# Performance work log

Measured on AMD Instinct MI355X. Metric: run time of the kernel, lower is better.

Reference implementation:

```python
import jax, jax.numpy as jnp
import numpy as np

B, N, D = 1024, 8192, 128
BETA = 0.25


def setup_inputs() -> dict:
    key = jax.random.key(0)
    kx, kw = jax.random.split(key)
    x = jax.random.normal(kx, (B, D), dtype=jnp.float32)
    # nn.Embedding weight init: uniform(-1/num_embeddings, 1/num_embeddings)
    W = jax.random.uniform(kw, (N, D), dtype=jnp.float32, minval=-1.0 / N, maxval=1.0 / N)
    return {"x": x, "W": W}


def reference(x, W):
    # Squared L2 distances: (B, N) via expansion; single GEMM for the cross term.
    dist = (x * x).sum(axis=1, keepdims=True) - 2.0 * (x @ W.T) + (W * W).sum(axis=1)[None, :]
    # (-dist).topk(k=1) == argmin(dist); torch keeps the k dim -> ind is (B, 1)
    ind = jnp.argmin(dist, axis=1)[:, None]
    q = W[ind]  # (B, 1, D) codebook gather (matches torch embedding(ind) shape)
    # Faithful to source: (B, D) broadcasts against (B, 1, D) -> (B, B, D)
    loss = BETA * jnp.mean((x - jax.lax.stop_gradient(q)) ** 2) + jnp.mean((jax.lax.stop_gradient(x) - q) ** 2)
    quantized = x + jax.lax.stop_gradient(q - x)  # straight-through; (B, B, D) per source broadcast
    return quantized, ind, loss
```

## Files before the change

kernel.cpp:

```cpp
#include <hip/hip_runtime.h>
#include <stdint.h>

typedef float vfloat4 __attribute__((ext_vector_type(4)));

static const long long QN       = 134217728LL;
static const long long IND_OFF  = QN;
static const long long LOSS_OFF = QN + 1024;

#define WS_W2    0
#define WS_X2    8192
#define WS_SX    9216
#define WS_SQ    9344
#define WS_SQ2   9472
#define WS_PVAL  16384
#define WS_PIDX  81920
#define WS_Q     147456

__global__ __launch_bounds__(256) void k_prep(const float* __restrict__ x,
                                              const float* __restrict__ W,
                                              float* __restrict__ ws) {
    const int b = blockIdx.x, tid = threadIdx.x;
    if (b < 36) {
        const float4* pr = (b < 32) ? ((const float4*)W + (size_t)(b * 256 + tid) * 32)
                                    : ((const float4*)x + (size_t)((b - 32) * 256 + tid) * 32);
        float s = 0.0f;
#pragma unroll 8
        for (int t = 0; t < 32; ++t) {
            float4 v = pr[t];
            s += v.x * v.x + v.y * v.y + v.z * v.z + v.w * v.w;
        }
        if (b < 32) ws[WS_W2 + b * 256 + tid] = s;
        else        ws[WS_X2 + (b - 32) * 256 + tid] = s;
    } else {
        __shared__ float sh[8][32];
        const int c = tid & 31, g = tid >> 5;
        const int col = (b - 36) * 32 + c;
        float sum = 0.0f;
        for (int r = g; r < 1024; r += 8) sum += x[(size_t)r * 128 + col];
        sh[g][c] = sum;
        __syncthreads();
        if (g == 0) {
            float t = 0.0f;
#pragma unroll
            for (int gg = 0; gg < 8; ++gg) t += sh[gg][c];
            ws[WS_SX + col] = t;
        }
        if (b == 36 && tid < 129) ws[WS_SQ + tid] = 0.0f;
    }
}

__global__ __launch_bounds__(256) void k_score(
    const float* __restrict__ x, const float* __restrict__ W,
    const float* __restrict__ w2, const float* __restrict__ x2,
    float* __restrict__ pval, int* __restrict__ pidx) {
    __shared__ float Xs[32][132];
    __shared__ float Wst[32][132];
    const int tid = threadIdx.x;
    const int tx = tid & 15, ty = tid >> 4;
    const int n0 = blockIdx.x * 128, m0 = blockIdx.y * 128;
    const float4* xv = (const float4*)x;
    const float4* wv = (const float4*)W;

    float acc[8][8];
#pragma unroll
    for (int i = 0; i < 8; ++i)
#pragma unroll
        for (int j = 0; j < 8; ++j) acc[i][j] = 0.0f;

    for (int kc = 0; kc < 4; ++kc) {
#pragma unroll
        for (int it = 0; it < 4; ++it) {
            int f = it * 256 + tid;
            int m = f >> 3, kq = f & 7;
            float4 a = xv[(size_t)(m0 + m) * 32 + kc * 8 + kq];
            float4 b = wv[(size_t)(n0 + m) * 32 + kc * 8 + kq];
            Xs[kq * 4 + 0][m] = a.x;
            Xs[kq * 4 + 1][m] = a.y;
            Xs[kq * 4 + 2][m] = a.z;
            Xs[kq * 4 + 3][m] = a.w;
            Wst[kq * 4 + 0][m] = b.x;
            Wst[kq * 4 + 1][m] = b.y;
            Wst[kq * 4 + 2][m] = b.z;
            Wst[kq * 4 + 3][m] = b.w;
        }
        __syncthreads();
#pragma unroll 8
        for (int k = 0; k < 32; ++k) {
            float4 a0 = *(const float4*)&Xs[k][ty * 8];
            float4 a1 = *(const float4*)&Xs[k][ty * 8 + 4];
            float4 b0 = *(const float4*)&Wst[k][tx * 8];
            float4 b1 = *(const float4*)&Wst[k][tx * 8 + 4];
            float af[8] = {a0.x, a0.y, a0.z, a0.w, a1.x, a1.y, a1.z, a1.w};
            float bf[8] = {b0.x, b0.y, b0.z, b0.w, b1.x, b1.y, b1.z, b1.w};
#pragma unroll
            for (int i = 0; i < 8; ++i)
#pragma unroll
                for (int j = 0; j < 8; ++j) acc[i][j] += af[i] * bf[j];
        }
        __syncthreads();
    }

    float w2v[8];
#pragma unroll
    for (int j = 0; j < 8; ++j) w2v[j] = w2[n0 + tx * 8 + j];

#pragma unroll
    for (int i = 0; i < 8; ++i) {
        const int row = m0 + ty * 8 + i;
        const float xxv = x2[row];
        float bestv;
        int besti = n0 + tx * 8;
        {
            float t = xxv - 2.0f * acc[i][0];
            bestv = t + w2v[0];
        }
#pragma unroll
        for (int j = 1; j < 8; ++j) {
            float t = xxv - 2.0f * acc[i][j];
            float s = t + w2v[j];
            if (s < bestv) { bestv = s; besti = n0 + tx * 8 + j; }
        }
        for (int off = 1; off < 16; off <<= 1) {
            float ov = __shfl_xor(bestv, off, 64);
            int oi = __shfl_xor(besti, off, 64);
            if (ov < bestv || (ov == bestv && oi < besti)) { bestv = ov; besti = oi; }
        }
        if (tx == 0) {
            pval[row * 64 + blockIdx.x] = bestv;
            pidx[row * 64 + blockIdx.x] = besti;
        }
    }
}

__global__ __launch_bounds__(256) void k_argmin(
    const float* __restrict__ W, const float* __restrict__ w2,
    const float* __restrict__ pval, const int* __restrict__ pidx,
    float* __restrict__ out, float* __restrict__ ws) {
    __shared__ int sidx[256];
    __shared__ float sh[2][128];
    const int tid = threadIdx.x;
    const int r = blockIdx.x * 256 + tid;
    float bestv = pval[r * 64];
    int besti = pidx[r * 64];
    for (int c = 1; c < 64; ++c) {
        float v = pval[r * 64 + c];
        if (v < bestv) { bestv = v; besti = pidx[r * 64 + c]; }
    }
    out[IND_OFF + r] = (float)besti;
    sidx[tid] = besti;

    float q2 = w2[besti];
    for (int off = 1; off < 64; off <<= 1) q2 += __shfl_xor(q2, off, 64);
    if ((tid & 63) == 0) atomicAdd(ws + WS_SQ2, q2);
    __syncthreads();

    const int c4 = tid & 31, rg = tid >> 5;
    float4* wsq = (float4*)(ws + WS_Q);
    const float4* wv = (const float4*)W;
#pragma unroll 4
    for (int it = 0; it < 32; ++it) {
        int rr = it * 8 + rg;
        int idx = sidx[rr];
        wsq[(size_t)(blockIdx.x * 256 + rr) * 32 + c4] = wv[(size_t)idx * 32 + c4];
    }

    const int d = tid & 127, g = tid >> 7;
    float s = 0.0f;
    for (int rr = g; rr < 256; rr += 2) s += W[(size_t)sidx[rr] * 128 + d];
    sh[g][d] = s;
    __syncthreads();
    if (g == 0) atomicAdd(ws + WS_SQ + d, sh[0][d] + sh[1][d]);
}

__global__ __launch_bounds__(256) void k_bcast(float* __restrict__ out,
                                               const float* __restrict__ ws) {
    const int bid = blockIdx.x, tid = threadIdx.x;
    if (bid == 0) {
        __shared__ float sh[256];
        float dotv = (tid < 128) ? ws[WS_SX + tid] * ws[WS_SQ + tid] : 0.0f;
        float sx2 = 0.0f;
        for (int r = tid; r < 1024; r += 256) sx2 += ws[WS_X2 + r];
        sh[tid] = dotv;
        __syncthreads();
        for (int s = 128; s > 0; s >>= 1) {
            if (tid < s) sh[tid] += sh[tid + s];
            __syncthreads();
        }
        const float dot = sh[0];
        __syncthreads();
        sh[tid] = sx2;
        __syncthreads();
        for (int s = 128; s > 0; s >>= 1) {
            if (tid < s) sh[tid] += sh[tid + s];
            __syncthreads();
        }
        if (tid == 0) {
            double Sx2 = (double)sh[0], Sq2 = (double)ws[WS_SQ2];
            double loss = 1.25 * (1024.0 * Sx2 + 1024.0 * Sq2 - 2.0 * (double)dot) / 134217728.0;
            out[LOSS_OFF] = (float)loss;
        }
        __syncthreads();
    }
    const int i = bid >> 3;
    const int e = bid & 7;
    const int t = tid & 31;
    const vfloat4* src = (const vfloat4*)(ws + WS_Q) + (size_t)i * 32;
    vfloat4 qv = src[t];
    vfloat4* dst = (vfloat4*)out + (size_t)i * 32768 + t;
    const int jend = e * 128 + 128;
    for (int j = e * 128 + (tid >> 5); j < jend; j += 8) {
        dst[(size_t)j * 32] = qv;
    }
}

extern "C" void kernel_launch(void* const* d_in, const int* in_sizes, int n_in,
                              void* d_out, int out_size, void* d_ws, size_t ws_size,
                              hipStream_t stream) {
    const float* x = (const float*)d_in[0];
    const float* W = (const float*)d_in[1];
    float* out = (float*)d_out;
    float* ws = (float*)d_ws;

    hipLaunchKernelGGL(k_prep, dim3(40), dim3(256), 0, stream, x, W, ws);
    hipLaunchKernelGGL(k_score, dim3(64, 8), dim3(256), 0, stream, x, W,
                       ws + WS_W2, ws + WS_X2, ws + WS_PVAL, (int*)(ws + WS_PIDX));
    hipLaunchKernelGGL(k_argmin, dim3(4), dim3(256), 0, stream, W, ws + WS_W2,
                       ws + WS_PVAL, (const int*)(ws + WS_PIDX), out, ws);
    hipLaunchKernelGGL(k_bcast, dim3(8192), dim3(256), 0, stream, out, ws);
}
```

Measured before the change: 638.7 us.

## Parallelize argmin reduction, use packed FMA in scoring, and batch broadcast blocks

The final argmin now uses one wavefront per row with shuffle reductions across 512 blocks, where before it used 4 blocks with a serial 64-element scan per thread. The loss sums (codebook row sums and squared norms) move into block 0 of the broadcast kernel, which removes the atomics. The score GEMM accumulates in float2 vectors via elementwise fma so the compiler can emit packed FMA instructions. The broadcast kernel now gives each block 4 chunks, using 2049 blocks instead of 8192, with a dedicated loss block that adds a serial 1024-row reduction.

New measurement: 770.5 us. 20.6% more time.

```diff
diff --git a/kernel.cpp b/kernel.cpp
--- a/kernel.cpp
+++ b/kernel.cpp
@@ -2,6 +2,7 @@
 #include <stdint.h>
 
 typedef float vfloat4 __attribute__((ext_vector_type(4)));
+typedef float vfloat2 __attribute__((ext_vector_type(2)));
 
 static const long long QN       = 134217728LL;
 static const long long IND_OFF  = QN;
@@ -10,8 +11,7 @@
 #define WS_W2    0
 #define WS_X2    8192
 #define WS_SX    9216
-#define WS_SQ    9344
-#define WS_SQ2   9472
+#define WS_IND   9344
 #define WS_PVAL  16384
 #define WS_PIDX  81920
 #define WS_Q     147456
@@ -45,10 +45,10 @@
             for (int gg = 0; gg < 8; ++gg) t += sh[gg][c];
             ws[WS_SX + col] = t;
         }
-        if (b == 36 && tid < 129) ws[WS_SQ + tid] = 0.0f;
-    }
-}
-
+    }
+}
+
+#define ACC(i, j) acc[i][(j) >> 1][(j) & 1]
 __global__ __launch_bounds__(256) void k_score(
     const float* __restrict__ x, const float* __restrict__ W,
     const float* __restrict__ w2, const float* __restrict__ x2,
@@ -61,11 +61,11 @@
     const float4* xv = (const float4*)x;
     const float4* wv = (const float4*)W;
 
-    float acc[8][8];
+    vfloat2 acc[8][4];
 #pragma unroll
     for (int i = 0; i < 8; ++i)
 #pragma unroll
-        for (int j = 0; j < 8; ++j) acc[i][j] = 0.0f;
+        for (int jp = 0; jp < 4; ++jp) acc[i][jp] = (vfloat2)(0.0f);
 
     for (int kc = 0; kc < 4; ++kc) {
 #pragma unroll
@@ -91,11 +91,19 @@
             float4 b0 = *(const float4*)&Wst[k][tx * 8];
             float4 b1 = *(const float4*)&Wst[k][tx * 8 + 4];
             float af[8] = {a0.x, a0.y, a0.z, a0.w, a1.x, a1.y, a1.z, a1.w};
-            float bf[8] = {b0.x, b0.y, b0.z, b0.w, b1.x, b1.y, b1.z, b1.w};
-#pragma unroll
-            for (int i = 0; i < 8; ++i)
-#pragma unroll
-                for (int j = 0; j < 8; ++j) acc[i][j] += af[i] * bf[j];
+            vfloat2 bb[4];
+            bb[0][0] = b0.x; bb[0][1] = b0.y;
+            bb[1][0] = b0.z; bb[1][1] = b0.w;
+            bb[2][0] = b1.x; bb[2][1] = b1.y;
+            bb[3][0] = b1.z; bb[3][1] = b1.w;
+#pragma unroll
+            for (int i = 0; i < 8; ++i) {
+                vfloat2 av;
+                av[0] = af[i]; av[1] = af[i];
+#pragma unroll
+                for (int jp = 0; jp < 4; ++jp)
+                    acc[i][jp] = __builtin_elementwise_fma(av, bb[jp], acc[i][jp]);
+            }
         }
         __syncthreads();
     }
@@ -111,12 +119,12 @@
         float bestv;
         int besti = n0 + tx * 8;
         {
-            float t = xxv - 2.0f * acc[i][0];
+            float t = xxv - 2.0f * ACC(i, 0);
             bestv = t + w2v[0];
         }
 #pragma unroll
         for (int j = 1; j < 8; ++j) {
-            float t = xxv - 2.0f * acc[i][j];
+            float t = xxv - 2.0f * ACC(i, j);
             float s = t + w2v[j];
             if (s < bestv) { bestv = s; besti = n0 + tx * 8 + j; }
         }
@@ -132,84 +140,91 @@
     }
 }
 
-__global__ __launch_bounds__(256) void k_argmin(
-    const float* __restrict__ W, const float* __restrict__ w2,
+__global__ __launch_bounds__(128) void k_argmin(
+    const float* __restrict__ W,
     const float* __restrict__ pval, const int* __restrict__ pidx,
     float* __restrict__ out, float* __restrict__ ws) {
-    __shared__ int sidx[256];
-    __shared__ float sh[2][128];
     const int tid = threadIdx.x;
-    const int r = blockIdx.x * 256 + tid;
-    float bestv = pval[r * 64];
-    int besti = pidx[r * 64];
-    for (int c = 1; c < 64; ++c) {
-        float v = pval[r * 64 + c];
-        if (v < bestv) { bestv = v; besti = pidx[r * 64 + c]; }
-    }
-    out[IND_OFF + r] = (float)besti;
-    sidx[tid] = besti;
-
-    float q2 = w2[besti];
-    for (int off = 1; off < 64; off <<= 1) q2 += __shfl_xor(q2, off, 64);
-    if ((tid & 63) == 0) atomicAdd(ws + WS_SQ2, q2);
-    __syncthreads();
-
-    const int c4 = tid & 31, rg = tid >> 5;
-    float4* wsq = (float4*)(ws + WS_Q);
-    const float4* wv = (const float4*)W;
-#pragma unroll 4
-    for (int it = 0; it < 32; ++it) {
-        int rr = it * 8 + rg;
-        int idx = sidx[rr];
-        wsq[(size_t)(blockIdx.x * 256 + rr) * 32 + c4] = wv[(size_t)idx * 32 + c4];
-    }
-
-    const int d = tid & 127, g = tid >> 7;
-    float s = 0.0f;
-    for (int rr = g; rr < 256; rr += 2) s += W[(size_t)sidx[rr] * 128 + d];
-    sh[g][d] = s;
-    __syncthreads();
-    if (g == 0) atomicAdd(ws + WS_SQ + d, sh[0][d] + sh[1][d]);
+    const int w = tid >> 6, lane = tid & 63;
+    const int r = blockIdx.x * 2 + w;
+    float bestv = pval[r * 64 + lane];
+    int besti = pidx[r * 64 + lane];
+    for (int off = 1; off < 64; off <<= 1) {
+        float ov = __shfl_xor(bestv, off, 64);
+        int oi = __shfl_xor(besti, off, 64);
+        if (ov < bestv || (ov == bestv && oi < besti)) { bestv = ov; besti = oi; }
+    }
+    if (lane == 0) {
+        out[IND_OFF + r] = (float)besti;
+        ((int*)ws)[WS_IND + r] = besti;
+    }
+    if (lane < 32) {
+        const float4* wv = (const float4*)W;
+        float4* wsq = (float4*)(ws + WS_Q);
+        wsq[(size_t)r * 32 + lane] = wv[(size_t)besti * 32 + lane];
+    }
 }
 
 __global__ __launch_bounds__(256) void k_bcast(float* __restrict__ out,
                                                const float* __restrict__ ws) {
     const int bid = blockIdx.x, tid = threadIdx.x;
     if (bid == 0) {
+        __shared__ float shq[2][128];
         __shared__ float sh[256];
-        float dotv = (tid < 128) ? ws[WS_SX + tid] * ws[WS_SQ + tid] : 0.0f;
+        const int d = tid & 127, g = tid >> 7;
+        float s = 0.0f;
+        for (int r = g; r < 1024; r += 2) s += ws[WS_Q + (size_t)r * 128 + d];
+        shq[g][d] = s;
+        __syncthreads();
+        float dotv = 0.0f;
+        if (tid < 128) dotv = (shq[0][tid] + shq[1][tid]) * ws[WS_SX + tid];
         float sx2 = 0.0f;
         for (int r = tid; r < 1024; r += 256) sx2 += ws[WS_X2 + r];
+        const int* wsI = (const int*)ws + WS_IND;
+        float sq2 = 0.0f;
+        for (int r = tid; r < 1024; r += 256) sq2 += ws[WS_W2 + wsI[r]];
         sh[tid] = dotv;
         __syncthreads();
-        for (int s = 128; s > 0; s >>= 1) {
-            if (tid < s) sh[tid] += sh[tid + s];
+        for (int st = 128; st > 0; st >>= 1) {
+            if (tid < st) sh[tid] += sh[tid + st];
             __syncthreads();
         }
         const float dot = sh[0];
         __syncthreads();
         sh[tid] = sx2;
         __syncthreads();
-        for (int s = 128; s > 0; s >>= 1) {
-            if (tid < s) sh[tid] += sh[tid + s];
+        for (int st = 128; st > 0; st >>= 1) {
+            if (tid < st) sh[tid] += sh[tid + st];
             __syncthreads();
         }
+        const float Sx2 = sh[0];
+        __syncthreads();
+        sh[tid] = sq2;
+        __syncthreads();
+        for (int st = 128; st > 0; st >>= 1) {
+            if (tid < st) sh[tid] += sh[tid + st];
+            __syncthreads();
+        }
         if (tid == 0) {
-            double Sx2 = (double)sh[0], Sq2 = (double)ws[WS_SQ2];
-            double loss = 1.25 * (1024.0 * Sx2 + 1024.0 * Sq2 - 2.0 * (double)dot) / 134217728.0;
+            double loss = 1.25 * (1024.0 * (double)Sx2 + 1024.0 * (double)sh[0] - 2.0 * (double)dot) / 134217728.0;
             out[LOSS_OFF] = (float)loss;
         }
-        __syncthreads();
-    }
-    const int i = bid >> 3;
-    const int e = bid & 7;
+        return;
+    }
+    const int c0 = (bid - 1) * 4;
     const int t = tid & 31;
-    const vfloat4* src = (const vfloat4*)(ws + WS_Q) + (size_t)i * 32;
-    vfloat4 qv = src[t];
-    vfloat4* dst = (vfloat4*)out + (size_t)i * 32768 + t;
-    const int jend = e * 128 + 128;
-    for (int j = e * 128 + (tid >> 5); j < jend; j += 8) {
-        dst[(size_t)j * 32] = qv;
+#pragma unroll
+    for (int cc = 0; cc < 4; ++cc) {
+        const int chunk = c0 + cc;
+        const int i = chunk >> 3;
+        const int e = chunk & 7;
+        const vfloat4* src = (const vfloat4*)(ws + WS_Q) + (size_t)i * 32;
+        vfloat4 qv = src[t];
+        vfloat4* dst = (vfloat4*)out + (size_t)i * 32768 + t;
+        const int jend = e * 128 + 128;
+        for (int j = e * 128 + (tid >> 5); j < jend; j += 8) {
+            dst[(size_t)j * 32] = qv;
+        }
     }
 }
 
@@ -224,7 +239,7 @@
     hipLaunchKernelGGL(k_prep, dim3(40), dim3(256), 0, stream, x, W, ws);
     hipLaunchKernelGGL(k_score, dim3(64, 8), dim3(256), 0, stream, x, W,
                        ws + WS_W2, ws + WS_X2, ws + WS_PVAL, (int*)(ws + WS_PIDX));
-    hipLaunchKernelGGL(k_argmin, dim3(4), dim3(256), 0, stream, W, ws + WS_W2,
+    hipLaunchKernelGGL(k_argmin, dim3(512), dim3(128), 0, stream, W,
                        ws + WS_PVAL, (const int*)(ws + WS_PIDX), out, ws);
-    hipLaunchKernelGGL(k_bcast, dim3(8192), dim3(256), 0, stream, out, ws);
-}
+    hipLaunchKernelGGL(k_bcast, dim3(2049), dim3(256), 0, stream, out, ws);
+}
```
